# Kernel tuning notes

Hardware: AMD Instinct MI355X
Metric: run time of the kernel (lower is better)

The kernel has to match this reference:

```python
import jax, jax.numpy as jnp
import numpy as np

NUM_HEADS = 12

def setup_inputs() -> dict:
    key = jax.random.key(0)
    k1, k2 = jax.random.split(key)
    X = jax.random.normal(k1, (2, 2048, 768), dtype=jnp.float32)
    # torch nn.Linear(dim, 2*dim, bias=False) weight has shape [2*dim, dim]
    W_qkv = jax.random.normal(k2, (1536, 768), dtype=jnp.float32) * (768 ** -0.5)
    return {"X": X, "W_qkv": W_qkv}

def reference(X, W_qkv):
    B, N, C = X.shape
    H = NUM_HEADS
    hd = C // H
    scale = hd ** -0.5
    # qkv: [B, N, 2, H, hd]
    qkv = (X @ W_qkv.T).reshape(B, N, 2, H, hd)
    q = jnp.transpose(qkv[:, :, 0], (0, 2, 1, 3))  # [B, H, N, hd]
    k = jnp.transpose(qkv[:, :, 1], (0, 2, 1, 3))  # [B, H, N, hd]
    attn = jnp.einsum('bhnd,bhmd->bhnm', q, k) * scale  # [B, H, N, N]
    # dropout p=0 -> identity; double sum over heads and keys
    scores = attn.sum(axis=1).sum(axis=-1)  # [B, N]
    return scores
```

## Files before the change

### kernel.cpp

```cpp
#include <hip/hip_runtime.h>


#define DIM 768
#define SEQ 2048
#define NGRP 8
#define NBLK 256
#define NB_B 128
#define PBASE 0xAAAAAAAAu


__global__ __launch_bounds__(256)
void fused_k(const float* __restrict__ X, const float* __restrict__ W,
             float* __restrict__ out, float* __restrict__ ws) {
    float* xpart = ws;
    float* t     = ws + 2 * NGRP * DIM;
    unsigned* cnt1 = (unsigned*)(ws + 16384);
    unsigned* cnt2 = cnt1 + 64;

    __shared__ alignas(16) float sbuf[DIM];
    __shared__ float vloc[12];
    __shared__ float red[3][16];

    const int bi   = blockIdx.x;
    const int tid  = threadIdx.x;
    const int lane = tid & 63;
    const int wv   = tid >> 6;

    const int b  = bi >> 7;
    const int ch = bi & 127;

    float4 xa[16];
    if (tid < 192) {
        const float4* base =
            (const float4*)(X + ((size_t)b * SEQ + (size_t)ch * 16) * DIM) + tid;
        float4 a0 = {0.f, 0.f, 0.f, 0.f};
        float4 a1 = {0.f, 0.f, 0.f, 0.f};
        #pragma unroll
        for (int n = 0; n < 16; n += 2) {
            xa[n]     = base[n * 192];
            xa[n + 1] = base[(n + 1) * 192];
            a0.x += xa[n].x;     a0.y += xa[n].y;
            a0.z += xa[n].z;     a0.w += xa[n].w;
            a1.x += xa[n + 1].x; a1.y += xa[n + 1].y;
            a1.z += xa[n + 1].z; a1.w += xa[n + 1].w;
        }
        a0.x += a1.x; a0.y += a1.y; a0.z += a1.z; a0.w += a1.w;
        int g = ch >> 4;
        float* dst = xpart + (size_t)(b * NGRP + g) * DIM + tid * 4;
        atomicAdd(dst + 0, a0.x);
        atomicAdd(dst + 1, a0.y);
        atomicAdd(dst + 2, a0.z);
        atomicAdd(dst + 3, a0.w);
    }
    __syncthreads();
    if (tid == 0)
        __hip_atomic_fetch_add(cnt1, 1u, __ATOMIC_RELAXED,
                               __HIP_MEMORY_SCOPE_AGENT);

    if (bi < NB_B) {
        int b2    = bi >> 6;
        int chunk = bi & 63;
        int c0    = chunk * 12;

        {
            const float4* wq4 = (const float4*)(W + (size_t)c0 * DIM);
            const float4* wk4 = (const float4*)(W + (size_t)(DIM + c0) * DIM);
            float dummy = 0.f;
            #pragma unroll
            for (int i = 0; i < 9; ++i) {
                float4 a = wq4[tid + i * 256];
                float4 c = wk4[tid + i * 256];
                dummy += a.x + a.w + c.x + c.w;
            }
            asm volatile("" :: "v"(dummy));
        }

        if (tid == 0) {
            int guard = 0;
            while (__hip_atomic_load(cnt1, __ATOMIC_RELAXED,
                                     __HIP_MEMORY_SCOPE_AGENT) != PBASE + NBLK) {
                __builtin_amdgcn_s_sleep(1);
                if (++guard > (1 << 24)) break;
            }
        }
        __syncthreads();

        #pragma unroll
        for (int k = 0; k < 3; ++k) {
            int d = tid + k * 256;
            const float* p = xpart + (size_t)(b2 * NGRP) * DIM + d;
            float s = 0.f;
            #pragma unroll
            for (int g = 0; g < NGRP; ++g)
                s += p[(size_t)g * DIM];
            sbuf[d] = s;
        }
        __syncthreads();

        const float4* xs4 = (const float4*)sbuf;
        #pragma unroll
        for (int ic = 0; ic < 3; ++ic) {
            int c = c0 + wv * 3 + ic;
            const float4* wr = (const float4*)(W + (size_t)(DIM + c) * DIM);
            float acc = 0.f;
            #pragma unroll
            for (int j = 0; j < 3; ++j) {
                float4 a = wr[lane + 64 * j];
                float4 s = xs4[lane + 64 * j];
                acc += a.x * s.x + a.y * s.y + a.z * s.z + a.w * s.w;
            }
            #pragma unroll
            for (int off = 32; off; off >>= 1) acc += __shfl_down(acc, off, 64);
            if (lane == 0) vloc[wv * 3 + ic] = acc;
        }
        __syncthreads();

        #pragma unroll
        for (int k = 0; k < 3; ++k) {
            int d = tid + k * 256;
            float acc = 0.f;
            #pragma unroll
            for (int i = 0; i < 12; ++i)
                acc += W[(size_t)(c0 + i) * DIM + d] * vloc[i];
            atomicAdd(&t[b2 * DIM + d], acc);
        }
        __syncthreads();
        if (tid == 0)
            __hip_atomic_fetch_add(cnt2, 1u, __ATOMIC_RELAXED,
                                   __HIP_MEMORY_SCOPE_AGENT);
    }

    if (tid == 0) {
        int guard = 0;
        while (__hip_atomic_load(cnt2, __ATOMIC_RELAXED,
                                 __HIP_MEMORY_SCOPE_AGENT) != PBASE + NB_B) {
            __builtin_amdgcn_s_sleep(4);
            if (++guard > (1 << 24)) break;
        }
    }
    __syncthreads();

    {
        if (tid < 192)
            ((float4*)sbuf)[tid] = ((const float4*)(t + b * DIM))[tid];
        __syncthreads();

        if (tid < 192) {
            float4 tv = ((const float4*)sbuf)[tid];
            float p[16];
            #pragma unroll
            for (int n = 0; n < 16; ++n)
                p[n] = xa[n].x * tv.x + xa[n].y * tv.y
                     + xa[n].z * tv.z + xa[n].w * tv.w;
            #pragma unroll
            for (int off = 32; off; off >>= 1) {
                #pragma unroll
                for (int n = 0; n < 16; ++n)
                    p[n] += __shfl_down(p[n], off, 64);
            }
            if (lane == 0) {
                #pragma unroll
                for (int n = 0; n < 16; ++n)
                    red[wv][n] = p[n];
            }
        }
        __syncthreads();
        if (tid < 16)
            out[bi * 16 + tid] =
                0.125f * (red[0][tid] + red[1][tid] + red[2][tid]);
    }
}

extern "C" void kernel_launch(void* const* d_in, const int* in_sizes, int n_in,
                              void* d_out, int out_size, void* d_ws, size_t ws_size,
                              hipStream_t stream) {
    const float* X = (const float*)d_in[0];
    const float* W = (const float*)d_in[1];
    float* out = (float*)d_out;
    float* ws  = (float*)d_ws;

    fused_k<<<NBLK, 256, 0, stream>>>(X, W, out, ws);
}
```

Before: 80.12 us.

## Split global barrier counters into per-batch, per-group cache-line counters

Replaces the single global arrival counters with separate counters for each batch and group, each padded onto its own cache line. Phase-2 blocks now wait only on the eight group counters of their own batch, and the final phase waits only on its batch's phase-2 counters. Phase-2 work moves to even-numbered blocks so both batches are handled by blocks spread across the grid. The aim is to cut atomic contention on one address and let each batch proceed without waiting for the other, at the cost of eight polling threads per block.

```diff
diff --git a/kernel.cpp b/kernel.cpp
--- a/kernel.cpp
+++ b/kernel.cpp
@@ -5,7 +5,6 @@
 #define SEQ 2048
 #define NGRP 8
 #define NBLK 256
-#define NB_B 128
 #define PBASE 0xAAAAAAAAu
 
 
@@ -14,8 +13,7 @@
              float* __restrict__ out, float* __restrict__ ws) {
     float* xpart = ws;
     float* t     = ws + 2 * NGRP * DIM;
-    unsigned* cnt1 = (unsigned*)(ws + 16384);
-    unsigned* cnt2 = cnt1 + 64;
+    unsigned* cw = (unsigned*)(ws + 16384);
 
     __shared__ alignas(16) float sbuf[DIM];
     __shared__ float vloc[12];
@@ -28,6 +26,7 @@
 
     const int b  = bi >> 7;
     const int ch = bi & 127;
+    const int g  = ch >> 4;
 
     float4 xa[16];
     if (tid < 192) {
@@ -45,7 +44,6 @@
             a1.z += xa[n + 1].z; a1.w += xa[n + 1].w;
         }
         a0.x += a1.x; a0.y += a1.y; a0.z += a1.z; a0.w += a1.w;
-        int g = ch >> 4;
         float* dst = xpart + (size_t)(b * NGRP + g) * DIM + tid * 4;
         atomicAdd(dst + 0, a0.x);
         atomicAdd(dst + 1, a0.y);
@@ -54,12 +52,11 @@
     }
     __syncthreads();
     if (tid == 0)
-        __hip_atomic_fetch_add(cnt1, 1u, __ATOMIC_RELAXED,
-                               __HIP_MEMORY_SCOPE_AGENT);
+        __hip_atomic_fetch_add(cw + (b * 8 + g) * 32, 1u,
+                               __ATOMIC_RELAXED, __HIP_MEMORY_SCOPE_AGENT);
 
-    if (bi < NB_B) {
-        int b2    = bi >> 6;
-        int chunk = bi & 63;
+    if ((bi & 1) == 0) {
+        int chunk = (bi >> 1) & 63;
         int c0    = chunk * 12;
 
         {
@@ -75,10 +72,11 @@
             asm volatile("" :: "v"(dummy));
         }
 
-        if (tid == 0) {
+        if (tid < 8) {
+            unsigned* line = cw + (b * 8 + tid) * 32;
             int guard = 0;
-            while (__hip_atomic_load(cnt1, __ATOMIC_RELAXED,
-                                     __HIP_MEMORY_SCOPE_AGENT) != PBASE + NBLK) {
+            while (__hip_atomic_load(line, __ATOMIC_RELAXED,
+                                     __HIP_MEMORY_SCOPE_AGENT) != PBASE + 16) {
                 __builtin_amdgcn_s_sleep(1);
                 if (++guard > (1 << 24)) break;
             }
@@ -88,11 +86,11 @@
         #pragma unroll
         for (int k = 0; k < 3; ++k) {
             int d = tid + k * 256;
-            const float* p = xpart + (size_t)(b2 * NGRP) * DIM + d;
+            const float* p = xpart + (size_t)(b * NGRP) * DIM + d;
             float s = 0.f;
             #pragma unroll
-            for (int g = 0; g < NGRP; ++g)
-                s += p[(size_t)g * DIM];
+            for (int gg = 0; gg < NGRP; ++gg)
+                s += p[(size_t)gg * DIM];
             sbuf[d] = s;
         }
         __syncthreads();
@@ -122,19 +120,20 @@
             #pragma unroll
             for (int i = 0; i < 12; ++i)
                 acc += W[(size_t)(c0 + i) * DIM + d] * vloc[i];
-            atomicAdd(&t[b2 * DIM + d], acc);
+            atomicAdd(&t[b * DIM + d], acc);
         }
         __syncthreads();
         if (tid == 0)
-            __hip_atomic_fetch_add(cnt2, 1u, __ATOMIC_RELAXED,
-                                   __HIP_MEMORY_SCOPE_AGENT);
+            __hip_atomic_fetch_add(cw + 512 + (b * 8 + (chunk >> 3)) * 32, 1u,
+                                   __ATOMIC_RELAXED, __HIP_MEMORY_SCOPE_AGENT);
     }
 
-    if (tid == 0) {
+    if (tid < 8) {
+        unsigned* line = cw + 512 + (b * 8 + tid) * 32;
         int guard = 0;
-        while (__hip_atomic_load(cnt2, __ATOMIC_RELAXED,
-                                 __HIP_MEMORY_SCOPE_AGENT) != PBASE + NB_B) {
-            __builtin_amdgcn_s_sleep(4);
+        while (__hip_atomic_load(line, __ATOMIC_RELAXED,
+                                 __HIP_MEMORY_SCOPE_AGENT) != PBASE + 8) {
+            __builtin_amdgcn_s_sleep(2);
             if (++guard > (1 << 24)) break;
         }
     }
```

Result: faster. 75.87 us (-5.3%).
